# Optimization experiments

Measured on AMD Instinct MI355X. Metric: run time of the kernel, lower is better.

## Reference

```python
import jax, jax.numpy as jnp
import numpy as np

N_NODES = 50000
N_EDGES = 600000
CLASSIC_DIM = 128
GRAPH_OUTPUT_DIM = 96
NUM_RELATIONS = 4


def setup_inputs() -> dict:
    key = jax.random.key(0)
    ks = jax.random.split(key, 10)
    x = jax.random.normal(ks[0], (N_NODES, CLASSIC_DIM), dtype=jnp.float32)
    edge_index = jax.random.randint(ks[1], (2, N_EDGES), 0, N_NODES, dtype=jnp.int64)
    edge_type = jax.random.randint(ks[2], (N_EDGES,), 0, NUM_RELATIONS, dtype=jnp.int64)
    s1 = 1.0 / np.sqrt(CLASSIC_DIM)
    W_root1 = jax.random.normal(ks[3], (CLASSIC_DIM, CLASSIC_DIM), dtype=jnp.float32) * s1
    W_rel1 = jax.random.normal(ks[4], (NUM_RELATIONS, CLASSIC_DIM, CLASSIC_DIM), dtype=jnp.float32) * s1
    b1 = jnp.zeros((CLASSIC_DIM,), dtype=jnp.float32)
    W_root2 = jax.random.normal(ks[5], (CLASSIC_DIM, GRAPH_OUTPUT_DIM), dtype=jnp.float32) * s1
    W_rel2 = jax.random.normal(ks[6], (NUM_RELATIONS, CLASSIC_DIM, GRAPH_OUTPUT_DIM), dtype=jnp.float32) * s1
    b2 = jnp.zeros((GRAPH_OUTPUT_DIM,), dtype=jnp.float32)
    return {"classic_features": x, "edge_index": edge_index, "edge_type": edge_type,
            "W_root1": W_root1, "W_rel1": W_rel1, "b1": b1,
            "W_root2": W_root2, "W_rel2": W_rel2, "b2": b2}


def _rgcn_layer(x, edge_index, edge_type, W_root, W_rel, b):
    # RGCN: h_i = W_root x_i + b + sum_r (1/deg_{i,r}) * W_r * sum_{j in N_r(i)} x_j
    # Aggregate-then-transform (valid by linearity) to keep the matmul small.
    src, dst = edge_index[0], edge_index[1]
    msgs = x[src]  # [E, d_in] irregular gather
    out = x @ W_root + b
    n = x.shape[0]
    num_rel = W_rel.shape[0]
    for r in range(num_rel):  # small fixed loop over relation types
        mask = (edge_type == r).astype(x.dtype)  # [E]
        agg = jax.ops.segment_sum(msgs * mask[:, None], dst, num_segments=n)  # [N, d_in]
        deg = jax.ops.segment_sum(mask, dst, num_segments=n)  # [N]
        agg = agg / jnp.maximum(deg, 1.0)[:, None]  # mean per relation (PyG default norm)
        out = out + agg @ W_rel[r]
    return out


def reference(classic_features, edge_index, edge_type, W_root1, W_rel1, b1, W_root2, W_rel2, b2):
    h = _rgcn_layer(classic_features, edge_index, edge_type, W_root1, W_rel1, b1)
    h = jax.nn.relu(h)
    # dropout(0.2) is identity in eval mode
    out = _rgcn_layer(h, edge_index, edge_type, W_root2, W_rel2, b2)
    return out
```

## Files before the change

### kernel.cpp

```cpp
#include <hip/hip_runtime.h>

#define DIM_IN 128
#define NREL 4
#define KTOT (DIM_IN + NREL * DIM_IN)
#define SCAN_CHUNK 1024

typedef __attribute__((ext_vector_type(8))) short short8;
typedef __attribute__((ext_vector_type(4))) float floatx4;

__device__ inline unsigned short f2bf(float f) {
    union { float f; unsigned int i; } c;
    c.f = f;
    unsigned int r = c.i + 0x7FFF + ((c.i >> 16) & 1);
    return (unsigned short)(r >> 16);
}
__device__ inline float bf2f(unsigned short u) {
    union { unsigned int i; float f; } c;
    c.i = ((unsigned int)u) << 16;
    return c.f;
}

__device__ inline void gload16_lds(const void* g, void* l) {
    __builtin_amdgcn_global_load_lds((const __attribute__((address_space(1))) unsigned int*)g,
                                     (__attribute__((address_space(3))) unsigned int*)l,
                                     16, 0, 0);
}

__global__ void count_kernel(const int* __restrict__ ei, const int* __restrict__ et,
                             int* __restrict__ counts, int E) {
    int e = blockIdx.x * 256 + threadIdx.x;
    if (e >= E) return;
    atomicAdd(&counts[(size_t)ei[E + e] * NREL + et[e]], 1);
}

__device__ int block_exscan256(int v) {
    __shared__ int tmp[256];
    int t = threadIdx.x;
    tmp[t] = v;
    __syncthreads();
    for (int d = 1; d < 256; d <<= 1) {
        int add = (t >= d) ? tmp[t - d] : 0;
        __syncthreads();
        tmp[t] += add;
        __syncthreads();
    }
    return tmp[t] - v;
}

__global__ __launch_bounds__(256) void scanA_kernel(const int* __restrict__ counts,
                                                    int* __restrict__ chunkTot, int nb) {
    int base = blockIdx.x * SCAN_CHUNK + threadIdx.x * 4;
    int s = 0;
#pragma unroll
    for (int i = 0; i < 4; i++) {
        int idx = base + i;
        s += (idx < nb) ? counts[idx] : 0;
    }
    __shared__ int red[256];
    red[threadIdx.x] = s;
    __syncthreads();
    for (int d = 128; d > 0; d >>= 1) {
        if (threadIdx.x < d) red[threadIdx.x] += red[threadIdx.x + d];
        __syncthreads();
    }
    if (threadIdx.x == 0) chunkTot[blockIdx.x] = red[0];
}

__global__ __launch_bounds__(256) void scanB_kernel(const int* __restrict__ chunkTot,
                                                    int* __restrict__ chunkBase, int nChunks) {
    int t = threadIdx.x;
    int v = (t < nChunks) ? chunkTot[t] : 0;
    int ex = block_exscan256(v);
    if (t < nChunks) chunkBase[t] = ex;
}

__global__ __launch_bounds__(256) void scanC_kernel(const int* __restrict__ counts,
                                                    const int* __restrict__ chunkBase,
                                                    int* __restrict__ offs,
                                                    int* __restrict__ cursor, int nb) {
    int base = blockIdx.x * SCAN_CHUNK + threadIdx.x * 4;
    int c[4], s = 0;
#pragma unroll
    for (int i = 0; i < 4; i++) {
        int idx = base + i;
        c[i] = (idx < nb) ? counts[idx] : 0;
        s += c[i];
    }
    int pos = block_exscan256(s) + chunkBase[blockIdx.x];
#pragma unroll
    for (int i = 0; i < 4; i++) {
        int idx = base + i;
        if (idx < nb) {
            offs[idx] = pos;
            cursor[idx] = pos;
        }
        pos += c[i];
    }
}

__global__ void place_kernel(const int* __restrict__ ei, const int* __restrict__ et,
                             int* __restrict__ cursor, int* __restrict__ csr, int E) {
    int e = blockIdx.x * 256 + threadIdx.x;
    if (e >= E) return;
    int b = ei[E + e] * NREL + et[e];
    int p = atomicAdd(&cursor[b], 1);
    csr[p] = ei[e];
}

__global__ void cvt_x_kernel(const float* __restrict__ x, unsigned short* __restrict__ xb,
                             int n4) {
    int i = blockIdx.x * 256 + threadIdx.x;
    if (i >= n4) return;
    float4 v = ((const float4*)x)[i];
    ushort4 o;
    o.x = f2bf(v.x); o.y = f2bf(v.y); o.z = f2bf(v.z); o.w = f2bf(v.w);
    ((ushort4*)xb)[i] = o;
}

template <int NOUT>
__global__ void cvt_w_kernel(const float* __restrict__ Wroot, const float* __restrict__ Wrel,
                             unsigned short* __restrict__ Wt) {
    int t = blockIdx.x * 256 + threadIdx.x;
    if (t >= NOUT * KTOT) return;
    int n = t / KTOT, k = t - n * KTOT;
    float v = (k < DIM_IN) ? Wroot[(size_t)k * NOUT + n]
                           : Wrel[(size_t)(k - DIM_IN) * NOUT + n];
    Wt[t] = f2bf(v);
}

__global__ __launch_bounds__(256) void agg_kernel(
    const unsigned short* __restrict__ feat, const int* __restrict__ csr,
    const int* __restrict__ offs, const int* __restrict__ counts,
    unsigned short* __restrict__ agg, int nb) {
    int l16 = threadIdx.x & 15;
    int g = (blockIdx.x * 256 + threadIdx.x) >> 4;
    if (g >= nb) return;
    int start = offs[g];
    int cnt = counts[g];
    float acc[8];
#pragma unroll
    for (int j = 0; j < 8; j++) acc[j] = 0.f;
    int i = 0;
    for (; i + 1 < cnt; i += 2) {
        int s0 = csr[start + i];
        int s1 = csr[start + i + 1];
        short8 u0 = *(const short8*)(feat + (size_t)s0 * DIM_IN + l16 * 8);
        short8 u1 = *(const short8*)(feat + (size_t)s1 * DIM_IN + l16 * 8);
#pragma unroll
        for (int j = 0; j < 8; j++)
            acc[j] += bf2f((unsigned short)u0[j]) + bf2f((unsigned short)u1[j]);
    }
    if (i < cnt) {
        int s0 = csr[start + i];
        short8 u0 = *(const short8*)(feat + (size_t)s0 * DIM_IN + l16 * 8);
#pragma unroll
        for (int j = 0; j < 8; j++) acc[j] += bf2f((unsigned short)u0[j]);
    }
    float sc = (cnt > 0) ? (1.0f / (float)cnt) : 0.f;
    short8 o;
#pragma unroll
    for (int j = 0; j < 8; j++) o[j] = (short)f2bf(acc[j] * sc);
    *(short8*)(agg + (size_t)g * DIM_IN + l16 * 8) = o;
}

template <int NOUT, bool STORE_BF16_RELU>
__global__ __launch_bounds__(256) void mfma_gemm_kernel(
    const unsigned short* __restrict__ xb,
    const unsigned short* __restrict__ agg,
    const unsigned short* __restrict__ Wt,
    const float* __restrict__ bias,
    void* __restrict__ outp,
    int N) {
    constexpr int NT = NOUT / 32;
    constexpr int BCHUNKS = NOUT * 4;
    __shared__ unsigned short sA[128 * 32];
    __shared__ unsigned short sB[NOUT * 32];
    const int t = threadIdx.x;
    const int w = t >> 6;
    const int lane = t & 63;
    const int q = lane >> 4;
    const int l15 = lane & 15;
    const int wm = w >> 1, wn = w & 1;
    const int m0 = blockIdx.x * 128;

    floatx4 acc[4][NT];
#pragma unroll
    for (int mt = 0; mt < 4; mt++)
#pragma unroll
        for (int nt = 0; nt < NT; nt++) acc[mt][nt] = (floatx4)0.f;

    for (int ks = 0; ks < KTOT / 32; ks++) {
        const int k0 = ks * 32;
#pragma unroll
        for (int r = 0; r < 2; r++) {
            int idx = t + r * 256;
            int row = idx >> 2, ch = idx & 3;
            int rowg = m0 + row;
            if (rowg >= N) rowg = N - 1;
            const unsigned short* gp =
                (k0 < DIM_IN)
                    ? (xb + (size_t)rowg * DIM_IN + k0 + ch * 8)
                    : (agg + (size_t)rowg * (NREL * DIM_IN) + (k0 - DIM_IN) + ch * 8);
            gload16_lds(gp, sA + (size_t)(r * 256 + w * 64) * 8);
        }
#pragma unroll
        for (int r = 0; r < (BCHUNKS + 255) / 256; r++) {
            if (r * 256 + w * 64 < BCHUNKS) {
                int idx = t + r * 256;
                int nrow = idx >> 2, ch = idx & 3;
                const unsigned short* gp = Wt + (size_t)nrow * KTOT + k0 + ch * 8;
                gload16_lds(gp, sB + (size_t)(r * 256 + w * 64) * 8);
            }
        }
        __syncthreads();
        short8 aF[4], bF[NT];
#pragma unroll
        for (int mt = 0; mt < 4; mt++)
            aF[mt] = *(const short8*)(sA + (size_t)(wm * 64 + mt * 16 + l15) * 32 + q * 8);
#pragma unroll
        for (int nt = 0; nt < NT; nt++)
            bF[nt] = *(const short8*)(sB + (size_t)(wn * (NOUT / 2) + nt * 16 + l15) * 32 + q * 8);
#pragma unroll
        for (int mt = 0; mt < 4; mt++)
#pragma unroll
            for (int nt = 0; nt < NT; nt++)
                acc[mt][nt] =
                    __builtin_amdgcn_mfma_f32_16x16x32_bf16(aF[mt], bF[nt], acc[mt][nt], 0, 0, 0);
        __syncthreads();
    }

#pragma unroll
    for (int nt = 0; nt < NT; nt++) {
        int colg = wn * (NOUT / 2) + nt * 16 + l15;
        float bv = bias[colg];
#pragma unroll
        for (int mt = 0; mt < 4; mt++) {
            int rbase = m0 + wm * 64 + mt * 16 + q * 4;
#pragma unroll
            for (int r = 0; r < 4; r++) {
                int grow = rbase + r;
                if (grow < N) {
                    float v = acc[mt][nt][r] + bv;
                    if (STORE_BF16_RELU) {
                        v = fmaxf(v, 0.f);
                        ((unsigned short*)outp)[(size_t)grow * NOUT + colg] = f2bf(v);
                    } else {
                        ((float*)outp)[(size_t)grow * NOUT + colg] = v;
                    }
                }
            }
        }
    }
}

extern "C" void kernel_launch(void* const* d_in, const int* in_sizes, int n_in,
                              void* d_out, int out_size, void* d_ws, size_t ws_size,
                              hipStream_t stream) {
    const float* x = (const float*)d_in[0];
    const int* ei = (const int*)d_in[1];
    const int* et = (const int*)d_in[2];
    const float* Wroot1 = (const float*)d_in[3];
    const float* Wrel1 = (const float*)d_in[4];
    const float* b1 = (const float*)d_in[5];
    const float* Wroot2 = (const float*)d_in[6];
    const float* Wrel2 = (const float*)d_in[7];
    const float* b2 = (const float*)d_in[8];
    float* out = (float*)d_out;

    int N = in_sizes[0] / DIM_IN;
    int E = in_sizes[2];
    int nb = N * NREL;
    int nChunks = (nb + SCAN_CHUNK - 1) / SCAN_CHUNK;

    char* p = (char*)d_ws;
    unsigned short* xb = (unsigned short*)p;   p += (size_t)N * DIM_IN * 2;
    unsigned short* hb = (unsigned short*)p;   p += (size_t)N * DIM_IN * 2;
    unsigned short* agg = (unsigned short*)p;  p += (size_t)nb * DIM_IN * 2;
    unsigned short* Wt1 = (unsigned short*)p;  p += (size_t)128 * KTOT * 2;
    unsigned short* Wt2 = (unsigned short*)p;  p += (size_t)96 * KTOT * 2;
    int* counts = (int*)p;                     p += (size_t)nb * 4;
    int* offs = (int*)p;                       p += (size_t)nb * 4;
    int* cursor = (int*)p;                     p += (size_t)nb * 4;
    int* chunkTot = (int*)p;                   p += 256 * 4;
    int* chunkBase = (int*)p;                  p += 256 * 4;
    int* csr = (int*)p;                        p += (size_t)E * 4;
    if ((size_t)(p - (char*)d_ws) > ws_size) return;

    hipMemsetAsync(counts, 0, (size_t)nb * sizeof(int), stream);
    count_kernel<<<(E + 255) / 256, 256, 0, stream>>>(ei, et, counts, E);
    scanA_kernel<<<nChunks, 256, 0, stream>>>(counts, chunkTot, nb);
    scanB_kernel<<<1, 256, 0, stream>>>(chunkTot, chunkBase, nChunks);
    scanC_kernel<<<nChunks, 256, 0, stream>>>(counts, chunkBase, offs, cursor, nb);
    place_kernel<<<(E + 255) / 256, 256, 0, stream>>>(ei, et, cursor, csr, E);

    int n4 = N * DIM_IN / 4;
    cvt_x_kernel<<<(n4 + 255) / 256, 256, 0, stream>>>(x, xb, n4);
    cvt_w_kernel<128><<<(128 * KTOT + 255) / 256, 256, 0, stream>>>(Wroot1, Wrel1, Wt1);
    cvt_w_kernel<96><<<(96 * KTOT + 255) / 256, 256, 0, stream>>>(Wroot2, Wrel2, Wt2);

    int gAgg = (nb * 16 + 255) / 256;
    int gB = (N + 127) / 128;
    agg_kernel<<<gAgg, 256, 0, stream>>>(xb, csr, offs, counts, agg, nb);
    mfma_gemm_kernel<128, true><<<gB, 256, 0, stream>>>(xb, agg, Wt1, b1, hb, N);
    agg_kernel<<<gAgg, 256, 0, stream>>>(hb, csr, offs, counts, agg, nb);
    mfma_gemm_kernel<96, false><<<gB, 256, 0, stream>>>(hb, agg, Wt2, b2, out, N);
}
```

Baseline: 269.9 us.

## Fuse prep kernels, shuffle-broadcast CSR indices in aggregation, double K-step in GEMM

Merges the x/weight bf16 conversion and edge-count kernels into one prep launch, which removes three launches. The aggregation kernel now loads up to 16 neighbor indices cooperatively and broadcasts them with shuffles instead of having every lane load each index. It also drops the two-way unroll. The GEMM processes two 32-wide K panels per barrier pair, which halves synchronizations at the cost of doubled LDS.

```diff
diff --git a/kernel.cpp b/kernel.cpp
--- a/kernel.cpp
+++ b/kernel.cpp
@@ -26,11 +26,38 @@
                                      16, 0, 0);
 }
 
-__global__ void count_kernel(const int* __restrict__ ei, const int* __restrict__ et,
-                             int* __restrict__ counts, int E) {
-    int e = blockIdx.x * 256 + threadIdx.x;
-    if (e >= E) return;
-    atomicAdd(&counts[(size_t)ei[E + e] * NREL + et[e]], 1);
+__global__ __launch_bounds__(256) void prep_kernel(
+    const float* __restrict__ x, unsigned short* __restrict__ xb, int n4,
+    const float* __restrict__ Wroot1, const float* __restrict__ Wrel1,
+    unsigned short* __restrict__ Wt1,
+    const float* __restrict__ Wroot2, const float* __restrict__ Wrel2,
+    unsigned short* __restrict__ Wt2,
+    const int* __restrict__ ei, const int* __restrict__ et,
+    int* __restrict__ counts, int E) {
+    int t = blockIdx.x * 256 + threadIdx.x;
+    if (t < n4) {
+        float4 v = ((const float4*)x)[t];
+        ushort4 o;
+        o.x = f2bf(v.x); o.y = f2bf(v.y); o.z = f2bf(v.z); o.w = f2bf(v.w);
+        ((ushort4*)xb)[t] = o;
+    }
+    if (t < (128 + 96) * KTOT) {
+        if (t < 128 * KTOT) {
+            int n = t / KTOT, k = t - n * KTOT;
+            float v = (k < DIM_IN) ? Wroot1[(size_t)k * 128 + n]
+                                   : Wrel1[(size_t)(k - DIM_IN) * 128 + n];
+            Wt1[t] = f2bf(v);
+        } else {
+            int t2 = t - 128 * KTOT;
+            int n = t2 / KTOT, k = t2 - n * KTOT;
+            float v = (k < DIM_IN) ? Wroot2[(size_t)k * 96 + n]
+                                   : Wrel2[(size_t)(k - DIM_IN) * 96 + n];
+            Wt2[t2] = f2bf(v);
+        }
+    }
+    if (t < E) {
+        atomicAdd(&counts[(size_t)ei[E + t] * NREL + et[t]], 1);
+    }
 }
 
 __device__ int block_exscan256(int v) {
@@ -105,27 +132,6 @@
     int b = ei[E + e] * NREL + et[e];
     int p = atomicAdd(&cursor[b], 1);
     csr[p] = ei[e];
-}
-
-__global__ void cvt_x_kernel(const float* __restrict__ x, unsigned short* __restrict__ xb,
-                             int n4) {
-    int i = blockIdx.x * 256 + threadIdx.x;
-    if (i >= n4) return;
-    float4 v = ((const float4*)x)[i];
-    ushort4 o;
-    o.x = f2bf(v.x); o.y = f2bf(v.y); o.z = f2bf(v.z); o.w = f2bf(v.w);
-    ((ushort4*)xb)[i] = o;
-}
-
-template <int NOUT>
-__global__ void cvt_w_kernel(const float* __restrict__ Wroot, const float* __restrict__ Wrel,
-                             unsigned short* __restrict__ Wt) {
-    int t = blockIdx.x * 256 + threadIdx.x;
-    if (t >= NOUT * KTOT) return;
-    int n = t / KTOT, k = t - n * KTOT;
-    float v = (k < DIM_IN) ? Wroot[(size_t)k * NOUT + n]
-                           : Wrel[(size_t)(k - DIM_IN) * NOUT + n];
-    Wt[t] = f2bf(v);
 }
 
 __global__ __launch_bounds__(256) void agg_kernel(
@@ -140,21 +146,17 @@
     float acc[8];
 #pragma unroll
     for (int j = 0; j < 8; j++) acc[j] = 0.f;
-    int i = 0;
-    for (; i + 1 < cnt; i += 2) {
-        int s0 = csr[start + i];
-        int s1 = csr[start + i + 1];
-        short8 u0 = *(const short8*)(feat + (size_t)s0 * DIM_IN + l16 * 8);
-        short8 u1 = *(const short8*)(feat + (size_t)s1 * DIM_IN + l16 * 8);
-#pragma unroll
-        for (int j = 0; j < 8; j++)
-            acc[j] += bf2f((unsigned short)u0[j]) + bf2f((unsigned short)u1[j]);
-    }
-    if (i < cnt) {
-        int s0 = csr[start + i];
-        short8 u0 = *(const short8*)(feat + (size_t)s0 * DIM_IN + l16 * 8);
-#pragma unroll
-        for (int j = 0; j < 8; j++) acc[j] += bf2f((unsigned short)u0[j]);
+    for (int base = 0; base < cnt; base += 16) {
+        int m = cnt - base;
+        if (m > 16) m = 16;
+        int pick = (l16 < m) ? l16 : (m - 1);
+        int idx = csr[start + base + pick];
+        for (int j = 0; j < m; j++) {
+            int s = __shfl(idx, j, 16);
+            short8 u = *(const short8*)(feat + (size_t)s * DIM_IN + l16 * 8);
+#pragma unroll
+            for (int c = 0; c < 8; c++) acc[c] += bf2f((unsigned short)u[c]);
+        }
     }
     float sc = (cnt > 0) ? (1.0f / (float)cnt) : 0.f;
     short8 o;
@@ -172,9 +174,12 @@
     void* __restrict__ outp,
     int N) {
     constexpr int NT = NOUT / 32;
-    constexpr int BCHUNKS = NOUT * 4;
-    __shared__ unsigned short sA[128 * 32];
-    __shared__ unsigned short sB[NOUT * 32];
+    constexpr int ACH = 128 * 8;
+    constexpr int BCH = NOUT * 8;
+    constexpr int APAN = 128 * 32;
+    constexpr int BPAN = NOUT * 32;
+    __shared__ unsigned short sA[2 * APAN];
+    __shared__ unsigned short sB[2 * BPAN];
     const int t = threadIdx.x;
     const int w = t >> 6;
     const int lane = t & 63;
@@ -189,43 +194,51 @@
 #pragma unroll
         for (int nt = 0; nt < NT; nt++) acc[mt][nt] = (floatx4)0.f;
 
-    for (int ks = 0; ks < KTOT / 32; ks++) {
-        const int k0 = ks * 32;
-#pragma unroll
-        for (int r = 0; r < 2; r++) {
+    for (int ks = 0; ks < KTOT / 64; ks++) {
+        const int k0 = ks * 64;
+#pragma unroll
+        for (int r = 0; r < ACH / 256; r++) {
             int idx = t + r * 256;
-            int row = idx >> 2, ch = idx & 3;
+            int panel = idx >> 9;
+            int rem = idx & 511;
+            int row = rem >> 2, ch = rem & 3;
             int rowg = m0 + row;
             if (rowg >= N) rowg = N - 1;
+            int col = panel * 32 + ch * 8;
             const unsigned short* gp =
                 (k0 < DIM_IN)
-                    ? (xb + (size_t)rowg * DIM_IN + k0 + ch * 8)
-                    : (agg + (size_t)rowg * (NREL * DIM_IN) + (k0 - DIM_IN) + ch * 8);
-            gload16_lds(gp, sA + (size_t)(r * 256 + w * 64) * 8);
-        }
-#pragma unroll
-        for (int r = 0; r < (BCHUNKS + 255) / 256; r++) {
-            if (r * 256 + w * 64 < BCHUNKS) {
-                int idx = t + r * 256;
-                int nrow = idx >> 2, ch = idx & 3;
-                const unsigned short* gp = Wt + (size_t)nrow * KTOT + k0 + ch * 8;
-                gload16_lds(gp, sB + (size_t)(r * 256 + w * 64) * 8);
-            }
-        }
-        __syncthreads();
-        short8 aF[4], bF[NT];
-#pragma unroll
-        for (int mt = 0; mt < 4; mt++)
-            aF[mt] = *(const short8*)(sA + (size_t)(wm * 64 + mt * 16 + l15) * 32 + q * 8);
-#pragma unroll
-        for (int nt = 0; nt < NT; nt++)
-            bF[nt] = *(const short8*)(sB + (size_t)(wn * (NOUT / 2) + nt * 16 + l15) * 32 + q * 8);
-#pragma unroll
-        for (int mt = 0; mt < 4; mt++)
+                    ? (xb + (size_t)rowg * DIM_IN + k0 + col)
+                    : (agg + (size_t)rowg * (NREL * DIM_IN) + (k0 - DIM_IN) + col);
+            gload16_lds(gp, sA + (size_t)idx * 8);
+        }
+#pragma unroll
+        for (int r = 0; r < BCH / 256; r++) {
+            int idx = t + r * 256;
+            int panel = idx / (NOUT * 4);
+            int rem = idx - panel * (NOUT * 4);
+            int nrow = rem >> 2, ch = rem & 3;
+            const unsigned short* gp = Wt + (size_t)nrow * KTOT + k0 + panel * 32 + ch * 8;
+            gload16_lds(gp, sB + (size_t)idx * 8);
+        }
+        __syncthreads();
+#pragma unroll
+        for (int s = 0; s < 2; s++) {
+            short8 aF[4], bF[NT];
+#pragma unroll
+            for (int mt = 0; mt < 4; mt++)
+                aF[mt] = *(const short8*)(sA + s * APAN +
+                                          (size_t)(wm * 64 + mt * 16 + l15) * 32 + q * 8);
 #pragma unroll
             for (int nt = 0; nt < NT; nt++)
-                acc[mt][nt] =
-                    __builtin_amdgcn_mfma_f32_16x16x32_bf16(aF[mt], bF[nt], acc[mt][nt], 0, 0, 0);
+                bF[nt] = *(const short8*)(sB + s * BPAN +
+                                          (size_t)(wn * (NOUT / 2) + nt * 16 + l15) * 32 + q * 8);
+#pragma unroll
+            for (int mt = 0; mt < 4; mt++)
+#pragma unroll
+                for (int nt = 0; nt < NT; nt++)
+                    acc[mt][nt] = __builtin_amdgcn_mfma_f32_16x16x32_bf16(aF[mt], bF[nt],
+                                                                          acc[mt][nt], 0, 0, 0);
+        }
         __syncthreads();
     }
 
@@ -286,17 +299,18 @@
     int* csr = (int*)p;                        p += (size_t)E * 4;
     if ((size_t)(p - (char*)d_ws) > ws_size) return;
 
+    int n4 = N * DIM_IN / 4;
+    int prepWork = n4;
+    if (prepWork < E) prepWork = E;
+    if (prepWork < (128 + 96) * KTOT) prepWork = (128 + 96) * KTOT;
+
     hipMemsetAsync(counts, 0, (size_t)nb * sizeof(int), stream);
-    count_kernel<<<(E + 255) / 256, 256, 0, stream>>>(ei, et, counts, E);
+    prep_kernel<<<(prepWork + 255) / 256, 256, 0, stream>>>(
+        x, xb, n4, Wroot1, Wrel1, Wt1, Wroot2, Wrel2, Wt2, ei, et, counts, E);
     scanA_kernel<<<nChunks, 256, 0, stream>>>(counts, chunkTot, nb);
     scanB_kernel<<<1, 256, 0, stream>>>(chunkTot, chunkBase, nChunks);
     scanC_kernel<<<nChunks, 256, 0, stream>>>(counts, chunkBase, offs, cursor, nb);
     place_kernel<<<(E + 255) / 256, 256, 0, stream>>>(ei, et, cursor, csr, E);
-
-    int n4 = N * DIM_IN / 4;
-    cvt_x_kernel<<<(n4 + 255) / 256, 256, 0, stream>>>(x, xb, n4);
-    cvt_w_kernel<128><<<(128 * KTOT + 255) / 256, 256, 0, stream>>>(Wroot1, Wrel1, Wt1);
-    cvt_w_kernel<96><<<(96 * KTOT + 255) / 256, 256, 0, stream>>>(Wroot2, Wrel2, Wt2);
 
     int gAgg = (nb * 16 + 255) / 256;
     int gB = (N + 127) / 128;
```

New measurement: 262.3 us. 2.8% less time.
